# Kernel optimization log

Hardware: AMD Instinct MI355X
Metric: run time of the kernel (lower is better)

Reference implementation:

```python
import jax, jax.numpy as jnp
import numpy as np

DIM = 256
HEADS = 8
G = 8            # group (window) size per axis
POS_DIM = 16     # (dim // 4) // 4
MLP_HIDDEN = 4 * DIM


def layernorm(x, g, b, eps=1e-5):
    m = x.mean(-1, keepdims=True)
    v = ((x - m) ** 2).mean(-1, keepdims=True)
    return (x - m) / jnp.sqrt(v + eps) * g + b


def setup_inputs() -> dict:
    key = jax.random.key(0)
    ks = jax.random.split(key, 32)
    s = 0.02
    d = {}
    d['x'] = jax.random.normal(ks[0], (1, 32768, DIM), jnp.float32)
    d['y'] = jax.random.normal(ks[1], (1, 32768, DIM), jnp.float32)
    d['n1_g'] = jnp.ones((DIM,), jnp.float32)
    d['n1_b'] = jnp.zeros((DIM,), jnp.float32)
    d['qkv_w'] = jax.random.normal(ks[2], (DIM, 3 * DIM), jnp.float32) * s
    d['qkv_b'] = jnp.zeros((3 * DIM,), jnp.float32)
    d['pp_w'] = jax.random.normal(ks[3], (3, POS_DIM), jnp.float32) * s
    d['pp_b'] = jnp.zeros((POS_DIM,), jnp.float32)
    d['p1_lng'] = jnp.ones((POS_DIM,), jnp.float32)
    d['p1_lnb'] = jnp.zeros((POS_DIM,), jnp.float32)
    d['p1_w'] = jax.random.normal(ks[4], (POS_DIM, POS_DIM), jnp.float32) * s
    d['p1_b'] = jnp.zeros((POS_DIM,), jnp.float32)
    d['p2_lng'] = jnp.ones((POS_DIM,), jnp.float32)
    d['p2_lnb'] = jnp.zeros((POS_DIM,), jnp.float32)
    d['p2_w'] = jax.random.normal(ks[5], (POS_DIM, POS_DIM), jnp.float32) * s
    d['p2_b'] = jnp.zeros((POS_DIM,), jnp.float32)
    d['p3_lng'] = jnp.ones((POS_DIM,), jnp.float32)
    d['p3_lnb'] = jnp.zeros((POS_DIM,), jnp.float32)
    d['p3_w'] = jax.random.normal(ks[6], (POS_DIM, HEADS), jnp.float32) * s
    d['p3_b'] = jnp.zeros((HEADS,), jnp.float32)
    d['proj_w'] = jax.random.normal(ks[7], (DIM, DIM), jnp.float32) * s
    d['proj_b'] = jnp.zeros((DIM,), jnp.float32)
    d['n2_g'] = jnp.ones((DIM,), jnp.float32)
    d['n2_b'] = jnp.zeros((DIM,), jnp.float32)
    d['fc1_w'] = jax.random.normal(ks[8], (DIM, MLP_HIDDEN), jnp.float32) * s
    d['fc1_b'] = jnp.zeros((MLP_HIDDEN,), jnp.float32)
    d['fc2_w'] = jax.random.normal(ks[9], (MLP_HIDDEN, DIM), jnp.float32) * s
    d['fc2_b'] = jnp.zeros((DIM,), jnp.float32)
    d['H'] = 32
    d['W'] = 32
    d['D'] = 32
    return d


def reference(x, y, n1_g, n1_b, qkv_w, qkv_b, pp_w, pp_b,
              p1_lng, p1_lnb, p1_w, p1_b, p2_lng, p2_lnb, p2_w, p2_b,
              p3_lng, p3_lnb, p3_w, p3_b, proj_w, proj_b,
              n2_g, n2_b, fc1_w, fc1_b, fc2_w, fc2_b, H, W, D):
    B, L, C = x.shape
    nh, g = HEADS, G
    hd = C // nh
    shortcut = x
    xn = layernorm(x, n1_g, n1_b)
    xv = xn.reshape(B, H, W, D, C)
    yv = y.reshape(B, H, W, D, C)  # note: y is NOT normed in the original

    # SDA window partition (H,W,D divisible by g -> no padding, zero mask)
    def part(t):
        t = t.reshape(B, H // g, g, W // g, g, D // g, g, C)
        t = t.transpose(0, 1, 3, 5, 2, 4, 6, 7)
        return t.reshape(-1, g * g * g, C)

    xg, yg = part(xv), part(yv)
    B_, N, _ = xg.shape

    # original quirk: self.qkv used for BOTH x and y (qkv_y layer unused)
    qkv = (xg @ qkv_w + qkv_b).reshape(B_, N, 3, nh, hd).transpose(2, 0, 3, 1, 4)
    qkv_y = (yg @ qkv_w + qkv_b).reshape(B_, N, 3, nh, hd).transpose(2, 0, 3, 1, 4)
    q = qkv[0] * (hd ** -0.5)
    k_y, v_y = qkv_y[1], qkv_y[2]

    attn = jnp.einsum('bhnd,bhmd->bhnm', q, k_y)  # [B_, nh, N, N]

    # dynamic relative position bias (small MLP + gather)
    rng = jnp.arange(1 - g, g)
    bh, bw, bd = jnp.meshgrid(rng, rng, rng, indexing='ij')
    biases = jnp.stack([bh, bw, bd], -1).reshape(-1, 3).astype(x.dtype)  # [(2g-1)^3, 3]
    pos = biases @ pp_w + pp_b
    pos = jax.nn.relu(layernorm(pos, p1_lng, p1_lnb)) @ p1_w + p1_b
    pos = jax.nn.relu(layernorm(pos, p2_lng, p2_lnb)) @ p2_w + p2_b
    pos = jax.nn.relu(layernorm(pos, p3_lng, p3_lnb)) @ p3_w + p3_b  # [(2g-1)^3, nh]

    c = jnp.arange(g)
    ch, cw, cd = jnp.meshgrid(c, c, c, indexing='ij')
    cf = jnp.stack([ch, cw, cd], 0).reshape(3, -1)          # [3, g^3]
    rel = (cf[:, :, None] - cf[:, None, :]).transpose(1, 2, 0) + (g - 1)
    idx = rel[..., 0] * (2 * g - 1) * (2 * g - 1) + rel[..., 1] * (2 * g - 1) + rel[..., 2]
    bias = pos[idx].transpose(2, 0, 1)  # [nh, N, N]

    attn = jax.nn.softmax(attn + bias[None], axis=-1)
    out = jnp.einsum('bhnm,bhmd->bhnd', attn, v_y).transpose(0, 2, 1, 3).reshape(B_, N, C)
    out = out @ proj_w + proj_b

    # reverse window partition
    out = out.reshape(B, H // g, W // g, D // g, g, g, g, C)
    out = out.transpose(0, 1, 4, 2, 5, 3, 6, 7).reshape(B, H * W * D, C)

    x = shortcut + out
    x2 = layernorm(x, n2_g, n2_b)
    h = jax.nn.gelu(x2 @ fc1_w + fc1_b, approximate=False)
    x = x + (h @ fc2_w + fc2_b)
    return x
```

## Files before the change

kernel.cpp:

```cpp
#include <hip/hip_runtime.h>
#include <cstdint>
#include <cstddef>

typedef unsigned int u32;
typedef unsigned short u16;
typedef __attribute__((ext_vector_type(8))) short bf16x8;
typedef __attribute__((ext_vector_type(4))) float f32x4;

#define DEV __device__ __forceinline__

DEV u16 f2b(float f){ u32 x = __float_as_uint(f); x += 0x7fffu + ((x>>16)&1u); return (u16)(x>>16); }
DEV u32 pk2(float a, float b){
  u32 r;
  asm("v_cvt_pk_bf16_f32 %0, %1, %2" : "=v"(r) : "v"(a), "v"(b));
  return r;
}

DEV void gll16(const void* g, void* l){
  __builtin_amdgcn_global_load_lds((const __attribute__((address_space(1))) u32*)g,
                                   (__attribute__((address_space(3))) u32*)l, 16, 0, 0);
}

DEV void win_n(int r, int& win, int& n){
  int d_ = r & 31, w_ = (r>>5)&31, h_ = r>>10;
  win = ((h_>>3)<<4) | ((w_>>3)<<2) | (d_>>3);
  n   = ((h_&7)<<6)  | ((w_&7)<<3)  | (d_&7);
}
DEV int tok_of(int r){
  int win = r>>9, nn = r&511;
  int bh = win>>4, bw=(win>>2)&3, bd=win&3;
  int ih = nn>>6,  iw=(nn>>3)&7,  id=nn&7;
  return ((bh*8+ih)<<10) | ((bw*8+iw)<<5) | (bd*8+id);
}


__global__ void wtrall_k(const float* __restrict__ qkv_w, const float* __restrict__ proj_w,
                         const float* __restrict__ fc1_w, const float* __restrict__ fc2_w,
                         u16* __restrict__ qkvT, u16* __restrict__ projT,
                         u16* __restrict__ fc1T, u16* __restrict__ fc2T){
  int f = blockIdx.x*256 + threadIdx.x;
  const float* w; u16* wt; int g; bool k10 = false; int N;
  if (f < 196608)      { w=qkv_w;  wt=qkvT;  g=f;        N=768;  }
  else if (f < 262144) { w=proj_w; wt=projT; g=f-196608; N=256;  }
  else if (f < 524288) { w=fc1_w;  wt=fc1T;  g=f-262144; N=1024; }
  else                 { w=fc2_w;  wt=fc2T;  g=f-524288; N=256;  k10=true; }
  int n = k10 ? (g>>10) : (g>>8);
  int k = k10 ? (g&1023) : (g&255);
  wt[g] = f2b(w[(size_t)k*N + n]);
}

__global__ void conv_k(const float* __restrict__ x, u16* __restrict__ o, int n4){
  int stride = gridDim.x*blockDim.x;
  for (int i = blockIdx.x*blockDim.x + threadIdx.x; i < n4; i += stride){
    const float4 v = *(const float4*)(x + (size_t)i*4);
    u32 lo = (u32)f2b(v.x) | ((u32)f2b(v.y)<<16);
    u32 hi = (u32)f2b(v.z) | ((u32)f2b(v.w)<<16);
    *(uint2*)(o + (size_t)i*4) = make_uint2(lo, hi);
  }
}

__global__ __launch_bounds__(256)
void ln_k(const float* __restrict__ x, const float* __restrict__ g,
          const float* __restrict__ b, u16* __restrict__ out){
  int row  = blockIdx.x*4 + (threadIdx.x>>6);
  int lane = threadIdx.x & 63;
  const float4 v = *(const float4*)(x + (size_t)row*256 + lane*4);
  float s = v.x+v.y+v.z+v.w;
  #pragma unroll
  for (int m=1;m<64;m<<=1) s += __shfl_xor(s, m);
  float mean = s * (1.0f/256.0f);
  float d0=v.x-mean,d1=v.y-mean,d2=v.z-mean,d3=v.w-mean;
  float q = d0*d0+d1*d1+d2*d2+d3*d3;
  #pragma unroll
  for (int m=1;m<64;m<<=1) q += __shfl_xor(q, m);
  float rs = rsqrtf(q*(1.0f/256.0f) + 1e-5f);
  const float4 gg = *(const float4*)(g + lane*4);
  const float4 bb = *(const float4*)(b + lane*4);
  u32 lo = (u32)f2b(d0*rs*gg.x+bb.x) | ((u32)f2b(d1*rs*gg.y+bb.y)<<16);
  u32 hi = (u32)f2b(d2*rs*gg.z+bb.z) | ((u32)f2b(d3*rs*gg.w+bb.w)<<16);
  *(uint2*)(out + (size_t)row*256 + lane*4) = make_uint2(lo,hi);
}

template<int NOUT>
DEV void pstage(float* v, const float* g, const float* b, const float* W, const float* bb){
  float m = 0.f;
  #pragma unroll
  for (int i=0;i<16;i++) m += v[i];
  m *= 0.0625f;
  float q = 0.f;
  #pragma unroll
  for (int i=0;i<16;i++){ float d=v[i]-m; q += d*d; }
  float rs = rsqrtf(q*0.0625f + 1e-5f);
  float u[16];
  #pragma unroll
  for (int i=0;i<16;i++){ float t = (v[i]-m)*rs*g[i] + b[i]; u[i] = t>0.f?t:0.f; }
  #pragma unroll
  for (int o=0;o<NOUT;o++){
    float s = bb[o];
    #pragma unroll
    for (int kk=0;kk<16;kk++) s += u[kk]*W[kk*NOUT+o];
    v[o] = s;
  }
}

__global__ void posmlp_k(const float* pp_w, const float* pp_b,
                         const float* g1, const float* b1, const float* w1, const float* bb1,
                         const float* g2, const float* b2, const float* w2, const float* bb2,
                         const float* g3, const float* b3, const float* w3, const float* bb3,
                         float* __restrict__ posb){
  int i = blockIdx.x*256 + threadIdx.x;
  if (i >= 3375) return;
  int t = i;
  int bd = t % 15; t /= 15;
  int bw = t % 15; t /= 15;
  int bh = t;
  float fh = (float)(bh-7), fw = (float)(bw-7), fd = (float)(bd-7);
  float v[16];
  #pragma unroll
  for (int o=0;o<16;o++) v[o] = fh*pp_w[o] + fw*pp_w[16+o] + fd*pp_w[32+o] + pp_b[o];
  pstage<16>(v, g1,b1,w1,bb1);
  pstage<16>(v, g2,b2,w2,bb2);
  pstage<8> (v, g3,b3,w3,bb3);
  #pragma unroll
  for (int h=0;h<8;h++) posb[(size_t)h*3376 + i] = v[h] * 1.4426950408889634f;
}

struct GemmP {
  const u16* A; const u16* Bt;
  int K;
  const float* bvec;
  float scale;
  const float* add32;
  float* out32;
  u16* out16;
  u16* out16b;
};

template<int MODE>
DEV void epi(const GemmP& p, int r, int c, float val){
  if constexpr (MODE==0){
    float qv = (val + p.bvec[c]) * p.scale;
    int win, n; win_n(r, win, n);
    int hh = c>>5, dd = c&31;
    p.out16[((size_t)((win*8+hh)*512 + n)<<5) + dd] = f2b(qv);
  } else if constexpr (MODE==1){
    float ov = val + p.bvec[c];
    int win, n; win_n(r, win, n);
    int cc = c & 255;
    int hh = cc>>5, dd = cc&31;
    size_t base = (size_t)(win*8+hh)*16384;
    if (c < 256){
      int nc = n>>4, ln2 = ((dd>>3)<<4)|(n&15), jj = dd&7;
      p.out16[base + (size_t)(nc*64+ln2)*8 + jj] = f2b(ov);
    } else {
      int fi = ((n>>5)<<1) | (dd>>4);
      int ln2 = (((n>>3)&3)<<4)|(dd&15), jj = n&7;
      p.out16b[base + (size_t)(fi*64+ln2)*8 + jj] = f2b(ov);
    }
  } else if constexpr (MODE==2){
    int l = tok_of(r);
    size_t o = (size_t)l*256 + c;
    p.out32[o] = val + p.bvec[c] + p.add32[o];
  } else if constexpr (MODE==3){
    float u = val + p.bvec[c];
    float ge = 0.5f*u*(1.0f + erff(u*0.70710678118654752f));
    p.out16[(size_t)r*1024 + c] = f2b(ge);
  } else {
    size_t o = (size_t)r*256 + c;
    p.out32[o] = val + p.bvec[c] + p.add32[o];
  }
}

template<int MODE, int NT>
__global__ __launch_bounds__(256)
void gemmA_k(GemmP p){
  __shared__ u16 lA[16384];
  __shared__ u16 lB[3][4096];
  const int tid = threadIdx.x;
  const int wid = tid>>6, lane = tid&63;
  const int lr = lane&15, lg = lane>>4;
  const int m0 = blockIdx.x*64;
  const int wm = (wid>>1)*32, wn = (wid&1)*64;
  const int T = NT*8;
  const f32x4 z4 = {0.f,0.f,0.f,0.f};

  #pragma unroll
  for (int it=0; it<8; ++it){
    int f = it*4 + wid;
    int rt = f>>3, kt = f&7;
    int row = m0 + rt*16 + lr;
    const u16* ga;
    if constexpr (MODE==2){
      ga = p.A + ((size_t)((row>>9)*8 + kt)*512 + (row&511))*32 + lg*8;
    } else {
      ga = p.A + (size_t)row*256 + kt*32 + lg*8;
    }
    gll16(ga, (char*)lA + f*1024 + lane*16);
  }
  auto stageB = [&](int buf, int t){
    int j = t>>3, kt = t&7;
    #pragma unroll
    for (int r=0;r<2;r++){
      int f = r*4 + wid;
      gll16(p.Bt + (size_t)(j*128 + f*16 + lr)*256 + kt*32 + lg*8,
            (char*)lB[buf] + f*1024 + lane*16);
    }
  };
  stageB(0, 0);
  if (T > 1) stageB(1, 1);

  f32x4 acc[2][4];
  #pragma unroll
  for (int i=0;i<2;i++)
    #pragma unroll
    for (int j=0;j<4;j++) acc[i][j] = z4;

  int cur = 0, stg = 2;
  for (int t=0; t<T; ++t){
    const int kt = t&7;
    if (t+1 < T) asm volatile("s_waitcnt vmcnt(2)" ::: "memory");
    else         asm volatile("s_waitcnt vmcnt(0)" ::: "memory");
    __builtin_amdgcn_s_barrier();
    __builtin_amdgcn_sched_barrier(0);
    bf16x8 af[2], bfr[4];
    #pragma unroll
    for (int i=0;i<2;i++){
      int fA = ((wid>>1)*2 + i)*8 + kt;
      af[i] = *(const bf16x8*)((const char*)lA + fA*1024 + lane*16);
    }
    #pragma unroll
    for (int j=0;j<4;j++){
      int fB = (wid&1)*4 + j;
      bfr[j] = *(const bf16x8*)((const char*)lB[cur] + fB*1024 + lane*16);
    }
    #pragma unroll
    for (int i=0;i<2;i++)
      #pragma unroll
      for (int j=0;j<4;j++)
        acc[i][j] = __builtin_amdgcn_mfma_f32_16x16x32_bf16(af[i], bfr[j], acc[i][j], 0,0,0);
    __builtin_amdgcn_sched_barrier(0);
    if (kt == 7){
      int n0 = (t>>3)*128;
      #pragma unroll
      for (int i=0;i<2;i++)
        #pragma unroll
        for (int j=0;j<4;j++){
          #pragma unroll
          for (int v=0;v<4;v++)
            epi<MODE>(p, m0 + wm + i*16 + lg*4 + v, n0 + wn + j*16 + lr, acc[i][j][v]);
          acc[i][j] = z4;
        }
    }
    if (t+2 < T) stageB(stg, t+2);
    cur = (cur==2)?0:cur+1;
    stg = (stg==2)?0:stg+1;
  }
}

__global__ __launch_bounds__(256)
void gemmW_k(GemmP p){
  __shared__ u16 lA[3][2048];
  __shared__ u16 lB[3][8192];
  const int tid = threadIdx.x;
  const int wid = tid>>6, lane = tid&63;
  const int lr = lane&15, lg = lane>>4;
  const int m0 = blockIdx.x*64;
  const int wm = (wid>>1)*32, wn = (wid&1)*128;
  const f32x4 z4 = {0.f,0.f,0.f,0.f};

  auto stage = [&](int buf, int kt){
    gll16(p.A + (size_t)(m0 + wid*16 + lr)*1024 + kt*32 + lg*8,
          (char*)lA[buf] + wid*1024 + lane*16);
    #pragma unroll
    for (int r=0;r<4;r++){
      int f = r*4 + wid;
      gll16(p.Bt + (size_t)(f*16 + lr)*1024 + kt*32 + lg*8,
            (char*)lB[buf] + f*1024 + lane*16);
    }
  };
  stage(0, 0);
  stage(1, 1);

  f32x4 acc[2][8];
  #pragma unroll
  for (int i=0;i<2;i++)
    #pragma unroll
    for (int j=0;j<8;j++) acc[i][j] = z4;

  int cur = 0, stg = 2;
  for (int kt=0; kt<32; ++kt){
    if (kt+1 < 32) asm volatile("s_waitcnt vmcnt(5)" ::: "memory");
    else           asm volatile("s_waitcnt vmcnt(0)" ::: "memory");
    __builtin_amdgcn_s_barrier();
    __builtin_amdgcn_sched_barrier(0);
    bf16x8 af[2], bfr[8];
    #pragma unroll
    for (int i=0;i<2;i++){
      int fA = (wid>>1)*2 + i;
      af[i] = *(const bf16x8*)((const char*)lA[cur] + fA*1024 + lane*16);
    }
    #pragma unroll
    for (int j=0;j<8;j++){
      int fB = (wid&1)*8 + j;
      bfr[j] = *(const bf16x8*)((const char*)lB[cur] + fB*1024 + lane*16);
    }
    #pragma unroll
    for (int i=0;i<2;i++)
      #pragma unroll
      for (int j=0;j<8;j++)
        acc[i][j] = __builtin_amdgcn_mfma_f32_16x16x32_bf16(af[i], bfr[j], acc[i][j], 0,0,0);
    __builtin_amdgcn_sched_barrier(0);
    if (kt+2 < 32) stage(stg, kt+2);
    cur = (cur==2)?0:cur+1;
    stg = (stg==2)?0:stg+1;
  }

  #pragma unroll
  for (int i=0;i<2;i++)
    #pragma unroll
    for (int j=0;j<8;j++)
      #pragma unroll
      for (int v=0;v<4;v++)
        epi<4>(p, m0 + wm + i*16 + lg*4 + v, wn + j*16 + lr, acc[i][j][v]);
}

__global__ __launch_bounds__(512, 2)
void attn_k(const u16* __restrict__ Q, const u16* __restrict__ Kf,
            const u16* __restrict__ Vf, const float* __restrict__ posb,
            u16* __restrict__ outF){
  __shared__ u16 lK[16384];
  __shared__ u16 lV[16384];
  __shared__ float lPf[3392];
  const int bid = blockIdx.x;
  const int hh = bid&7;
  const int tid = threadIdx.x, wid = tid>>6, lane = tid&63;
  const int lr = lane&15, lg = lane>>4;
  const u16* Kb = Kf + (size_t)bid*16384;
  const u16* Vb = Vf + (size_t)bid*16384;
  const u16* Qb = Q  + (size_t)bid*16384;
  #pragma unroll
  for (int r=0;r<4;r++){
    int off = (r*512 + tid)*16;
    gll16((const char*)Kb + off, (char*)lK + off);
    gll16((const char*)Vb + off, (char*)lV + off);
  }
  const float* ptab = posb + (size_t)hh*3376;
  for (int t=tid; t<3375; t+=512) lPf[t] = ptab[t];
  __syncthreads();
  const f32x4 z4 = {0.f,0.f,0.f,0.f};

  for (int ch=0; ch<4; ++ch){
    const int r0 = wid*64 + ch*16;
    const int q  = r0 + lr;
    const int Ab = (q>>6)*225 + ((q>>3)&7)*15 + (q&7) + 1687 - (lg>>1)*15 - (lg&1)*4;
    bf16x8 qf = *(const bf16x8*)(Qb + (size_t)q*32 + lg*8);
    f32x4 o0 = z4, o1 = z4;
    float sv0 = 0.f, sv1 = 0.f, sv2 = 0.f, sv3 = 0.f;
    #pragma unroll
    for (int ph=0; ph<2; ++ph){
      f32x4 sf[16];
      __builtin_amdgcn_s_setprio(1);
      #pragma unroll
      for (int i=0;i<16;i++){
        int nc = ph*16 + i;
        bf16x8 kf = *(const bf16x8*)&lK[(nc*64 + lane)*8];
        sf[i] = __builtin_amdgcn_mfma_f32_16x16x32_bf16(kf, qf, z4, 0,0,0);
      }
      __builtin_amdgcn_s_setprio(0);
      #pragma unroll
      for (int i=0;i<16;i++){
        int nc = ph*16 + i;
        const float* bp = lPf + (Ab - (nc>>2)*225 - (nc&3)*30 - 3);
        float e3 = exp2f(sf[i][3] + bp[0]);
        float e2 = exp2f(sf[i][2] + bp[1]);
        float e1 = exp2f(sf[i][1] + bp[2]);
        float e0 = exp2f(sf[i][0] + bp[3]);
        sf[i][0]=e0; sf[i][1]=e1; sf[i][2]=e2; sf[i][3]=e3;
        sv0 += e0; sv1 += e1; sv2 += e2; sv3 += e3;
      }
      #pragma unroll
      for (int kc=0;kc<8;kc++){
        u32 a0 = pk2(sf[2*kc  ][0], sf[2*kc  ][1]);
        u32 a1 = pk2(sf[2*kc  ][2], sf[2*kc  ][3]);
        u32 b0 = pk2(sf[2*kc+1][0], sf[2*kc+1][1]);
        u32 b1 = pk2(sf[2*kc+1][2], sf[2*kc+1][3]);
        asm("v_permlane32_swap_b32 %0, %1" : "+v"(a0), "+v"(b0));
        asm("v_permlane16_swap_b32 %0, %1" : "+v"(a0), "+v"(b0));
        asm("v_permlane32_swap_b32 %0, %1" : "+v"(a1), "+v"(b1));
        asm("v_permlane16_swap_b32 %0, %1" : "+v"(a1), "+v"(b1));
        bf16x8 pf;
        ((u32*)&pf)[0]=a0; ((u32*)&pf)[1]=a1; ((u32*)&pf)[2]=b0; ((u32*)&pf)[3]=b1;
        int kcg = ph*8 + kc;
        bf16x8 v0 = *(const bf16x8*)&lV[(size_t)((kcg*2+0)*64 + lane)*8];
        bf16x8 v1 = *(const bf16x8*)&lV[(size_t)((kcg*2+1)*64 + lane)*8];
        __builtin_amdgcn_s_setprio(1);
        o0 = __builtin_amdgcn_mfma_f32_16x16x32_bf16(pf, v0, o0, 0,0,0);
        o1 = __builtin_amdgcn_mfma_f32_16x16x32_bf16(pf, v1, o1, 0,0,0);
        __builtin_amdgcn_s_setprio(0);
      }
    }
    float s = (sv0+sv1) + (sv2+sv3);
    s += __shfl_xor(s,16);
    s += __shfl_xor(s,32);
    #pragma unroll
    for (int v=0;v<4;v++){
      float inv = 1.0f / __shfl(s, lg*4+v);
      int n = r0 + lg*4 + v;
      size_t base = ((size_t)bid*512 + n)*32;
      outF[base + lr]      = f2b(o0[v]*inv);
      outF[base + 16 + lr] = f2b(o1[v]*inv);
    }
  }
}

extern "C" void kernel_launch(void* const* d_in, const int* in_sizes, int n_in,
                              void* d_out, int out_size, void* d_ws, size_t ws_size,
                              hipStream_t stream){
  const float* x      = (const float*)d_in[0];
  const float* y      = (const float*)d_in[1];
  const float* n1_g   = (const float*)d_in[2];
  const float* n1_b   = (const float*)d_in[3];
  const float* qkv_w  = (const float*)d_in[4];
  const float* qkv_b  = (const float*)d_in[5];
  const float* pp_w   = (const float*)d_in[6];
  const float* pp_b   = (const float*)d_in[7];
  const float* p1_lng = (const float*)d_in[8];
  const float* p1_lnb = (const float*)d_in[9];
  const float* p1_w   = (const float*)d_in[10];
  const float* p1_b   = (const float*)d_in[11];
  const float* p2_lng = (const float*)d_in[12];
  const float* p2_lnb = (const float*)d_in[13];
  const float* p2_w   = (const float*)d_in[14];
  const float* p2_b   = (const float*)d_in[15];
  const float* p3_lng = (const float*)d_in[16];
  const float* p3_lnb = (const float*)d_in[17];
  const float* p3_w   = (const float*)d_in[18];
  const float* p3_b   = (const float*)d_in[19];
  const float* proj_w = (const float*)d_in[20];
  const float* proj_b = (const float*)d_in[21];
  const float* n2_g   = (const float*)d_in[22];
  const float* n2_b   = (const float*)d_in[23];
  const float* fc1_w  = (const float*)d_in[24];
  const float* fc1_b  = (const float*)d_in[25];
  const float* fc2_w  = (const float*)d_in[26];
  const float* fc2_b  = (const float*)d_in[27];
  float* out = (float*)d_out;
  char* ws = (char*)d_ws;

  u16*   qkvT  = (u16*)  (ws + 0);
  u16*   projT = (u16*)  (ws + 393216);
  u16*   fc1T  = (u16*)  (ws + 524288);
  u16*   fc2T  = (u16*)  (ws + 1048576);
  float* posb  = (float*)(ws + 1572864);
  u16*   xn    = (u16*)  (ws + 5898240);
  u16*   yb    = (u16*)  (ws + 22675456);
  u16*   Qb    = (u16*)  (ws + 39452672);
  u16*   Kfb   = (u16*)  (ws + 56229888);
  u16*   Vfb   = (u16*)  (ws + 73007104);
  u16*   attnF = (u16*)  (ws + 89784320);
  float* xres  = (float*)(ws + 106561536);
  u16*   hbuf  = xn;
  u16*   x2n   = attnF;

  wtrall_k<<<3072,256,0,stream>>>(qkv_w, proj_w, fc1_w, fc2_w, qkvT, projT, fc1T, fc2T);
  posmlp_k<<<14,256,0,stream>>>(pp_w, pp_b,
                                p1_lng,p1_lnb,p1_w,p1_b,
                                p2_lng,p2_lnb,p2_w,p2_b,
                                p3_lng,p3_lnb,p3_w,p3_b, posb);
  ln_k<<<8192,256,0,stream>>>(x, n1_g, n1_b, xn);
  conv_k<<<2048,256,0,stream>>>(y, yb, 2097152);

  GemmP pq; pq.A=xn; pq.Bt=qkvT; pq.K=256; pq.bvec=qkv_b;
  pq.scale=0.17677669529663687f*1.4426950408889634f;
  pq.add32=nullptr; pq.out32=nullptr; pq.out16=Qb; pq.out16b=nullptr;
  gemmA_k<0,2><<<512,256,0,stream>>>(pq);

  GemmP pkv; pkv.A=yb; pkv.Bt=qkvT + 256*256; pkv.K=256; pkv.bvec=qkv_b + 256;
  pkv.scale=1.f; pkv.add32=nullptr; pkv.out32=nullptr; pkv.out16=Kfb; pkv.out16b=Vfb;
  gemmA_k<1,4><<<512,256,0,stream>>>(pkv);

  attn_k<<<512,512,0,stream>>>(Qb, Kfb, Vfb, posb, attnF);

  GemmP pp; pp.A=attnF; pp.Bt=projT; pp.K=256; pp.bvec=proj_b;
  pp.scale=1.f; pp.add32=x; pp.out32=xres; pp.out16=nullptr; pp.out16b=nullptr;
  gemmA_k<2,2><<<512,256,0,stream>>>(pp);

  ln_k<<<8192,256,0,stream>>>(xres, n2_g, n2_b, x2n);

  GemmP pf1; pf1.A=x2n; pf1.Bt=fc1T; pf1.K=256; pf1.bvec=fc1_b;
  pf1.scale=1.f; pf1.add32=nullptr; pf1.out32=nullptr; pf1.out16=hbuf; pf1.out16b=nullptr;
  gemmA_k<3,8><<<512,256,0,stream>>>(pf1);

  GemmP pf2; pf2.A=hbuf; pf2.Bt=fc2T; pf2.K=1024; pf2.bvec=fc2_b;
  pf2.scale=1.f; pf2.add32=xres; pf2.out32=out; pf2.out16=nullptr; pf2.out16b=nullptr;
  gemmW_k<<<512,256,0,stream>>>(pf2);
}
```

Before: 292.5 us.

## Use 8-wave GEMM blocks and fast sigmoid-based GELU approximation

```diff
diff --git a/kernel.cpp b/kernel.cpp
--- a/kernel.cpp
+++ b/kernel.cpp
@@ -163,7 +163,8 @@
     p.out32[o] = val + p.bvec[c] + p.add32[o];
   } else if constexpr (MODE==3){
     float u = val + p.bvec[c];
-    float ge = 0.5f*u*(1.0f + erff(u*0.70710678118654752f));
+    float e = exp2f(u*(2.3022083f + 0.1029437f*u*u));
+    float ge = u*e*__builtin_amdgcn_rcpf(e+1.f);
     p.out16[(size_t)r*1024 + c] = f2b(ge);
   } else {
     size_t o = (size_t)r*256 + c;
@@ -172,7 +173,7 @@
 }
 
 template<int MODE, int NT>
-__global__ __launch_bounds__(256)
+__global__ __launch_bounds__(512, 2)
 void gemmA_k(GemmP p){
   __shared__ u16 lA[16384];
   __shared__ u16 lB[3][4096];
@@ -180,13 +181,13 @@
   const int wid = tid>>6, lane = tid&63;
   const int lr = lane&15, lg = lane>>4;
   const int m0 = blockIdx.x*64;
-  const int wm = (wid>>1)*32, wn = (wid&1)*64;
+  const int wm = (wid>>2)*32, wn = (wid&3)*32;
   const int T = NT*8;
   const f32x4 z4 = {0.f,0.f,0.f,0.f};
 
   #pragma unroll
-  for (int it=0; it<8; ++it){
-    int f = it*4 + wid;
+  for (int it=0; it<4; ++it){
+    int f = it*8 + wid;
     int rt = f>>3, kt = f&7;
     int row = m0 + rt*16 + lr;
     const u16* ga;
@@ -199,44 +200,39 @@
   }
   auto stageB = [&](int buf, int t){
     int j = t>>3, kt = t&7;
-    #pragma unroll
-    for (int r=0;r<2;r++){
-      int f = r*4 + wid;
-      gll16(p.Bt + (size_t)(j*128 + f*16 + lr)*256 + kt*32 + lg*8,
-            (char*)lB[buf] + f*1024 + lane*16);
-    }
+    gll16(p.Bt + (size_t)(j*128 + wid*16 + lr)*256 + kt*32 + lg*8,
+          (char*)lB[buf] + wid*1024 + lane*16);
   };
   stageB(0, 0);
   if (T > 1) stageB(1, 1);
 
-  f32x4 acc[2][4];
-  #pragma unroll
-  for (int i=0;i<2;i++)
-    #pragma unroll
-    for (int j=0;j<4;j++) acc[i][j] = z4;
+  f32x4 acc[2][2];
+  #pragma unroll
+  for (int i=0;i<2;i++){ acc[i][0]=z4; acc[i][1]=z4; }
 
   int cur = 0, stg = 2;
   for (int t=0; t<T; ++t){
     const int kt = t&7;
-    if (t+1 < T) asm volatile("s_waitcnt vmcnt(2)" ::: "memory");
-    else         asm volatile("s_waitcnt vmcnt(0)" ::: "memory");
+    if (t+1 >= T)          asm volatile("s_waitcnt vmcnt(0)"  ::: "memory");
+    else if (kt==0 && t)   asm volatile("s_waitcnt vmcnt(17)" ::: "memory");
+    else                   asm volatile("s_waitcnt vmcnt(1)"  ::: "memory");
     __builtin_amdgcn_s_barrier();
     __builtin_amdgcn_sched_barrier(0);
-    bf16x8 af[2], bfr[4];
+    bf16x8 af[2], bfr[2];
     #pragma unroll
     for (int i=0;i<2;i++){
-      int fA = ((wid>>1)*2 + i)*8 + kt;
+      int fA = ((wid>>2)*2 + i)*8 + kt;
       af[i] = *(const bf16x8*)((const char*)lA + fA*1024 + lane*16);
     }
     #pragma unroll
-    for (int j=0;j<4;j++){
-      int fB = (wid&1)*4 + j;
+    for (int j=0;j<2;j++){
+      int fB = (wid&3)*2 + j;
       bfr[j] = *(const bf16x8*)((const char*)lB[cur] + fB*1024 + lane*16);
     }
     #pragma unroll
     for (int i=0;i<2;i++)
       #pragma unroll
-      for (int j=0;j<4;j++)
+      for (int j=0;j<2;j++)
         acc[i][j] = __builtin_amdgcn_mfma_f32_16x16x32_bf16(af[i], bfr[j], acc[i][j], 0,0,0);
     __builtin_amdgcn_sched_barrier(0);
     if (kt == 7){
@@ -244,7 +240,7 @@
       #pragma unroll
       for (int i=0;i<2;i++)
         #pragma unroll
-        for (int j=0;j<4;j++){
+        for (int j=0;j<2;j++){
           #pragma unroll
           for (int v=0;v<4;v++)
             epi<MODE>(p, m0 + wm + i*16 + lg*4 + v, n0 + wn + j*16 + lr, acc[i][j][v]);
@@ -257,7 +253,7 @@
   }
 }
 
-__global__ __launch_bounds__(256)
+__global__ __launch_bounds__(512, 2)
 void gemmW_k(GemmP p){
   __shared__ u16 lA[3][2048];
   __shared__ u16 lB[3][8192];
@@ -265,49 +261,55 @@
   const int wid = tid>>6, lane = tid&63;
   const int lr = lane&15, lg = lane>>4;
   const int m0 = blockIdx.x*64;
-  const int wm = (wid>>1)*32, wn = (wid&1)*128;
+  const int wm = (wid>>2)*32, wn = (wid&3)*64;
   const f32x4 z4 = {0.f,0.f,0.f,0.f};
 
   auto stage = [&](int buf, int kt){
-    gll16(p.A + (size_t)(m0 + wid*16 + lr)*1024 + kt*32 + lg*8,
-          (char*)lA[buf] + wid*1024 + lane*16);
-    #pragma unroll
-    for (int r=0;r<4;r++){
-      int f = r*4 + wid;
-      gll16(p.Bt + (size_t)(f*16 + lr)*1024 + kt*32 + lg*8,
-            (char*)lB[buf] + f*1024 + lane*16);
+    {
+      int f = wid>>1, half = wid&1;
+      if (lane < 32){
+        int lg2 = half*2 + (lane>>4);
+        gll16(p.A + (size_t)(m0 + f*16 + (lane&15))*1024 + kt*32 + lg2*8,
+              (char*)lA[buf] + f*1024 + half*512 + lane*16);
+      }
+    }
+    #pragma unroll
+    for (int r=0;r<2;r++){
+      int fb = wid*2 + r;
+      gll16(p.Bt + (size_t)(fb*16 + lr)*1024 + kt*32 + lg*8,
+            (char*)lB[buf] + fb*1024 + lane*16);
     }
   };
   stage(0, 0);
   stage(1, 1);
 
-  f32x4 acc[2][8];
+  f32x4 acc[2][4];
   #pragma unroll
   for (int i=0;i<2;i++)
     #pragma unroll
-    for (int j=0;j<8;j++) acc[i][j] = z4;
+    for (int j=0;j<4;j++) acc[i][j] = z4;
 
   int cur = 0, stg = 2;
   for (int kt=0; kt<32; ++kt){
-    if (kt+1 < 32) asm volatile("s_waitcnt vmcnt(5)" ::: "memory");
+    if (kt+1 < 32) asm volatile("s_waitcnt vmcnt(3)" ::: "memory");
     else           asm volatile("s_waitcnt vmcnt(0)" ::: "memory");
     __builtin_amdgcn_s_barrier();
     __builtin_amdgcn_sched_barrier(0);
-    bf16x8 af[2], bfr[8];
+    bf16x8 af[2], bfr[4];
     #pragma unroll
     for (int i=0;i<2;i++){
-      int fA = (wid>>1)*2 + i;
+      int fA = (wid>>2)*2 + i;
       af[i] = *(const bf16x8*)((const char*)lA[cur] + fA*1024 + lane*16);
     }
     #pragma unroll
-    for (int j=0;j<8;j++){
-      int fB = (wid&1)*8 + j;
+    for (int j=0;j<4;j++){
+      int fB = (wid&3)*4 + j;
       bfr[j] = *(const bf16x8*)((const char*)lB[cur] + fB*1024 + lane*16);
     }
     #pragma unroll
     for (int i=0;i<2;i++)
       #pragma unroll
-      for (int j=0;j<8;j++)
+      for (int j=0;j<4;j++)
         acc[i][j] = __builtin_amdgcn_mfma_f32_16x16x32_bf16(af[i], bfr[j], acc[i][j], 0,0,0);
     __builtin_amdgcn_sched_barrier(0);
     if (kt+2 < 32) stage(stg, kt+2);
@@ -318,7 +320,7 @@
   #pragma unroll
   for (int i=0;i<2;i++)
     #pragma unroll
-    for (int j=0;j<8;j++)
+    for (int j=0;j<4;j++)
       #pragma unroll
       for (int v=0;v<4;v++)
         epi<4>(p, m0 + wm + i*16 + lg*4 + v, wn + j*16 + lr, acc[i][j][v]);
@@ -473,25 +475,25 @@
   GemmP pq; pq.A=xn; pq.Bt=qkvT; pq.K=256; pq.bvec=qkv_b;
   pq.scale=0.17677669529663687f*1.4426950408889634f;
   pq.add32=nullptr; pq.out32=nullptr; pq.out16=Qb; pq.out16b=nullptr;
-  gemmA_k<0,2><<<512,256,0,stream>>>(pq);
+  gemmA_k<0,2><<<512,512,0,stream>>>(pq);
 
   GemmP pkv; pkv.A=yb; pkv.Bt=qkvT + 256*256; pkv.K=256; pkv.bvec=qkv_b + 256;
   pkv.scale=1.f; pkv.add32=nullptr; pkv.out32=nullptr; pkv.out16=Kfb; pkv.out16b=Vfb;
-  gemmA_k<1,4><<<512,256,0,stream>>>(pkv);
+  gemmA_k<1,4><<<512,512,0,stream>>>(pkv);
 
   attn_k<<<512,512,0,stream>>>(Qb, Kfb, Vfb, posb, attnF);
 
   GemmP pp; pp.A=attnF; pp.Bt=projT; pp.K=256; pp.bvec=proj_b;
   pp.scale=1.f; pp.add32=x; pp.out32=xres; pp.out16=nullptr; pp.out16b=nullptr;
-  gemmA_k<2,2><<<512,256,0,stream>>>(pp);
+  gemmA_k<2,2><<<512,512,0,stream>>>(pp);
 
   ln_k<<<8192,256,0,stream>>>(xres, n2_g, n2_b, x2n);
 
   GemmP pf1; pf1.A=x2n; pf1.Bt=fc1T; pf1.K=256; pf1.bvec=fc1_b;
   pf1.scale=1.f; pf1.add32=nullptr; pf1.out32=nullptr; pf1.out16=hbuf; pf1.out16b=nullptr;
-  gemmA_k<3,8><<<512,256,0,stream>>>(pf1);
+  gemmA_k<3,8><<<512,512,0,stream>>>(pf1);
 
   GemmP pf2; pf2.A=hbuf; pf2.Bt=fc2T; pf2.K=1024; pf2.bvec=fc2_b;
   pf2.scale=1.f; pf2.add32=xres; pf2.out32=out; pf2.out16=nullptr; pf2.out16b=nullptr;
-  gemmW_k<<<512,256,0,stream>>>(pf2);
-}
+  gemmW_k<<<512,512,0,stream>>>(pf2);
+}
```

New measurement: 270.6 us. 1.08x faster.
